# Kernel tuning notes

Measured on AMD Instinct MI355X. Metric: run time of the kernel, lower is better.

## Reference

```python
import jax, jax.numpy as jnp
import numpy as np

# Fixed hyperparameters from init_kwargs
KH, KW = 3, 3
GRID_SIZE = 5
SPLINE_ORDER = 3
GRID_RANGE = (-1.0, 1.0)


def _make_grid():
    # grid buffer: arange(-k, grid_size + k + 1) * h + grid_range[0], shape (G + 2k + 1,) = (12,)
    h = (GRID_RANGE[1] - GRID_RANGE[0]) / GRID_SIZE
    return (jnp.arange(-SPLINE_ORDER, GRID_SIZE + SPLINE_ORDER + 1, dtype=jnp.float32) * h
            + GRID_RANGE[0])


def _unfold(x):
    # torch.nn.Unfold with kernel (3,3), stride 1, pad 0, dilation 1.
    # Returns (N, C*KH*KW) with channel-major ordering (c, i, j), matching torch.
    B, C, H, W = x.shape
    Ho, Wo = H - KH + 1, W - KW + 1
    cols = [x[:, :, i:i + Ho, j:j + Wo] for i in range(KH) for j in range(KW)]
    p = jnp.stack(cols, axis=2)                    # (B, C, KH*KW, Ho, Wo)
    p = p.reshape(B, C * KH * KW, Ho * Wo)         # (B, in_features, L)
    p = p.transpose(0, 2, 1).reshape(-1, C * KH * KW)  # (B*L, in_features)
    return p, Ho, Wo


def _b_splines(x, grid):
    # x: (N, in_features); grid: (G + 2k + 1,) uniform, shared across features.
    # Returns (N, in_features, G + k) B-spline basis via Cox-de Boor recursion.
    x = x[..., None]  # (N, in, 1)
    bases = ((x >= grid[:-1]) & (x < grid[1:])).astype(x.dtype)  # (N, in, G+2k)
    for k in range(1, SPLINE_ORDER + 1):
        left = (x - grid[: -(k + 1)]) / (grid[k:-1] - grid[: -(k + 1)])
        right = (grid[k + 1:] - x) / (grid[k + 1:] - grid[1:-k])
        bases = left * bases[..., :-1] + right * bases[..., 1:]
    return bases  # (N, in, G + k)


def setup_inputs() -> dict:
    key = jax.random.key(0)
    k1, k2, k3, k4 = jax.random.split(key, 4)
    in_features = 32 * KH * KW  # 288
    out_features = 64
    n_coef = GRID_SIZE + SPLINE_ORDER  # 8
    x = jax.random.normal(k1, (16, 32, 64, 64), dtype=jnp.float32)
    base_weight = jax.random.normal(k2, (out_features, in_features), dtype=jnp.float32) * (1.0 / np.sqrt(in_features))
    spline_weight = jax.random.normal(k3, (out_features, in_features, n_coef), dtype=jnp.float32) * 0.1
    spline_scaler = jax.random.normal(k4, (out_features, in_features), dtype=jnp.float32) * (1.0 / np.sqrt(in_features))
    return {"x": x, "base_weight": base_weight, "spline_weight": spline_weight,
            "spline_scaler": spline_scaler}


def reference(x, base_weight, spline_weight, spline_scaler):
    B = x.shape[0]
    out_features = base_weight.shape[0]
    grid = _make_grid()

    patches, Ho, Wo = _unfold(x)                              # (N, in_features)
    N, in_features = patches.shape

    # KANLinear forward
    base_out = jnp.matmul(jax.nn.relu(patches), base_weight.T)  # (N, out)
    bases = _b_splines(patches, grid)                           # (N, in, G+k)
    scaled_w = spline_weight * spline_scaler[..., None]         # (out, in, G+k)
    spline_out = jnp.matmul(bases.reshape(N, -1), scaled_w.reshape(out_features, -1).T)
    out = base_out + spline_out                                 # (N, out)

    out = out.reshape(B, Ho, Wo, out_features).transpose(0, 3, 1, 2)  # (B, C_out, Ho, Wo)
    return out
```

## Files before the change

### kernel.cpp

```cpp
#include <hip/hip_runtime.h>
#include <stdint.h>

typedef _Float16 half8  __attribute__((ext_vector_type(8)));
typedef float    f32x4  __attribute__((ext_vector_type(4)));
typedef uint32_t u32x4  __attribute__((ext_vector_type(4)));

#define FIN  288
#define NOUT 64
#define LPB  3844
#define KSPL 72
#define SC   200
#define LDSN (31*SC + 2*64 + 64 + 8)


__global__ void prep_bfrag(const float* __restrict__ bw,
                           const float* __restrict__ sw,
                           const float* __restrict__ sc,
                           half8* __restrict__ bfrag) {
  int t = blockIdx.x * 256 + threadIdx.x;
  half8 v;
  int dst;
  if (t < NOUT * FIN) {
    int o = t / FIN;
    int f = t - o * FIN;
    float scale = sc[t];
    const float* p = sw + t * 8;
#pragma unroll
    for (int c = 0; c < 8; ++c) v[c] = (_Float16)(p[c] * scale);
    int ch = f / 9;
    int r  = f - ch * 9;
    int ii = r / 3;
    int jj = r - ii * 3;
    int g  = ch >> 2, q = ch & 3;
    int kt = ii * 24 + jj * 8 + g;
    dst = (kt * 4 + (o >> 4)) * 64 + q * 16 + (o & 15);
  } else {
    int t2 = t - NOUT * FIN;
    int lane = t2 & 63;
    int nf = (t2 >> 6) & 3;
    int ktb = t2 >> 8;
    int o = nf * 16 + (lane & 15);
    int f0 = ktb * 32 + (lane >> 4) * 8;
    const float* p = bw + o * FIN + f0;
#pragma unroll
    for (int c = 0; c < 8; ++c) v[c] = (_Float16)p[c];
    dst = ((KSPL + ktb) * 4 + nf) * 64 + lane;
  }
  bfrag[dst] = v;
}

__device__ inline half8 bspline8(float xv) {
  float u = fmaf(xv, 2.5f, 5.5f);
  float fi = floorf(u);
  int i = (int)fi;
  float t = u - fi, s = 1.0f - t;
  float t2 = t * t, t3 = t2 * t;
  float s2 = s * s, s3 = s2 * s;
  float w3 = t3 * 0.16666667f;
  float w0 = s3 * 0.16666667f;
  float w1 = fmaf(0.5f, t3, -t2) + 0.66666667f;
  float w2 = fmaf(0.5f, s3, -s2) + 0.66666667f;
  uint32_t u01 = __builtin_bit_cast(uint32_t, __builtin_amdgcn_cvt_pkrtz(w0, w1));
  uint32_t u23 = __builtin_bit_cast(uint32_t, __builtin_amdgcn_cvt_pkrtz(w2, w3));
  uint64_t V = (uint64_t)u01 | ((uint64_t)u23 << 32);
  uint32_t vl = (uint32_t)(V << 16);
  u32x4 fr;
#pragma unroll
  for (int q = 0; q < 4; ++q) {
    int d = i - 2 * q;
    uint32_t rr = (uint32_t)(V >> ((48 - 16 * d) & 63));
    fr[q] = ((uint32_t)d <= 3u) ? rr : ((d == 4) ? vl : 0u);
  }
  return __builtin_bit_cast(half8, fr);
}

__global__ __launch_bounds__(256, 4) void kan_main(
    const float* __restrict__ x,
    const half8* __restrict__ bfrag,
    float* __restrict__ out) {
  __shared__ float lx[LDSN];

  const int tid = threadIdx.x;
  const int bid = blockIdx.x;
  const int b  = bid / 62;
  const int ho = bid - b * 62;

  const float* xb = x + b * 131072 + ho * 64;
#pragma unroll
  for (int r = 0; r < 6; ++r) {
    int gid = r * 256 + tid;
    int row = gid >> 4;
    int c   = (row * 683) >> 11;
    int ii  = row - c * 3;
    int colv = (gid & 15) * 4;
    const float4 v = *(const float4*)(xb + c * 4096 + ii * 64 + colv);
    *(float4*)(&lx[c * SC + ii * 64 + colv]) = v;
  }
  __syncthreads();

  const int lane = tid & 63;
  const int wv   = tid >> 6;
  const int quad = lane >> 4;
  const int m16  = lane & 15;
  const int wo   = wv * 16 + m16;

  f32x4 acc[4];
#pragma unroll
  for (int nf = 0; nf < 4; ++nf) acc[nf] = (f32x4){0.f, 0.f, 0.f, 0.f};

  int kt = 0;
#pragma unroll
  for (int ii = 0; ii < 3; ++ii) {
#pragma unroll
    for (int jj = 0; jj < 3; ++jj) {
      const float* lbase = lx + quad * SC + ii * 64 + wo + jj;
#pragma unroll
      for (int g = 0; g < 8; ++g) {
        float xv = lbase[g * (4 * SC)];
        half8 af = bspline8(xv);
#pragma unroll
        for (int nf = 0; nf < 4; ++nf) {
          half8 bf = bfrag[(kt * 4 + nf) * 64 + lane];
          acc[nf] = __builtin_amdgcn_mfma_f32_16x16x32_f16(af, bf, acc[nf], 0, 0, 0);
        }
        ++kt;
      }
    }
  }

#pragma unroll
  for (int kb = 0; kb < 9; ++kb) {
    int f0 = kb * 32 + quad * 8;
    half8 a;
#pragma unroll
    for (int j = 0; j < 8; ++j) {
      int f = f0 + j;
      int c = (f * 57) >> 9;
      int r = f - c * 9;
      int i2 = (r * 11) >> 5;
      int j2 = r - i2 * 3;
      a[j] = (_Float16)fmaxf(lx[c * SC + i2 * 64 + wo + j2], 0.0f);
    }
#pragma unroll
    for (int nf = 0; nf < 4; ++nf) {
      half8 bf = bfrag[((KSPL + kb) * 4 + nf) * 64 + lane];
      acc[nf] = __builtin_amdgcn_mfma_f32_16x16x32_f16(a, bf, acc[nf], 0, 0, 0);
    }
  }

  float* ob = out + b * (NOUT * LPB) + ho * 62;
#pragma unroll
  for (int rg = 0; rg < 4; ++rg) {
    int wo2 = wv * 16 + quad * 4 + rg;
    if (wo2 < 62) {
#pragma unroll
      for (int nf = 0; nf < 4; ++nf) {
        int o = nf * 16 + m16;
        ob[o * LPB + wo2] = acc[nf][rg];
      }
    }
  }
}

extern "C" void kernel_launch(void* const* d_in, const int* in_sizes, int n_in,
                              void* d_out, int out_size, void* d_ws, size_t ws_size,
                              hipStream_t stream) {
  const float* x  = (const float*)d_in[0];
  const float* bw = (const float*)d_in[1];
  const float* sw = (const float*)d_in[2];
  const float* sc = (const float*)d_in[3];
  float* out = (float*)d_out;
  half8* bfrag = (half8*)d_ws;

  prep_bfrag<<<81, 256, 0, stream>>>(bw, sw, sc, bfrag);
  kan_main<<<16 * 62, 256, 0, stream>>>(x, bfrag, out);
}
```

Measured before the change: 121.3 us.

## Precompute B-spline bases in a separate pass and restructure GEMM with 32x32 MFMA tiles

Adds a kernel that evaluates the cubic B-spline basis once per input element and writes the half8 results to workspace. The main kernel is rewritten as a 128-pixel-tile GEMM using 32x32x16 MFMAs with weights as the A operand. Weight chunks are double-buffered in LDS through global_load_lds, and the basis vectors are read directly from global memory. This removes the nine-fold redundant basis evaluation per pixel, but adds a 32 MB intermediate write and read plus an extra launch. The grid also shrinks to 481 blocks of 128 threads, which may underfill the device.

New measurement: 145.3 us. 19.8% more time.

```diff
diff --git a/kernel.cpp b/kernel.cpp
--- a/kernel.cpp
+++ b/kernel.cpp
@@ -2,51 +2,51 @@
 #include <stdint.h>
 
 typedef _Float16 half8  __attribute__((ext_vector_type(8)));
-typedef float    f32x4  __attribute__((ext_vector_type(4)));
+typedef float    f32x16 __attribute__((ext_vector_type(16)));
 typedef uint32_t u32x4  __attribute__((ext_vector_type(4)));
 
-#define FIN  288
+#define NPIX 61504
+#define LPB  3844
 #define NOUT 64
-#define LPB  3844
-#define KSPL 72
-#define SC   200
-#define LDSN (31*SC + 2*64 + 64 + 8)
-
-
-__global__ void prep_bfrag(const float* __restrict__ bw,
-                           const float* __restrict__ sw,
-                           const float* __restrict__ sc,
-                           half8* __restrict__ bfrag) {
+#define NXPIX 2097152
+#define WTAB_HALF8 20736
+#define BFRAG_BYTES 332800
+#define WS_NEED ((size_t)BFRAG_BYTES + (size_t)NXPIX * 16)
+
+
+__global__ void prep_w(const float* __restrict__ bw,
+                       const float* __restrict__ sw,
+                       const float* __restrict__ sc,
+                       half8* __restrict__ wt) {
   int t = blockIdx.x * 256 + threadIdx.x;
   half8 v;
-  int dst;
-  if (t < NOUT * FIN) {
-    int o = t / FIN;
-    int f = t - o * FIN;
+  int fi, h, o;
+  if (t < 64 * 288) {
+    o = t / 288;
+    int f = t - o * 288;
     float scale = sc[t];
     const float* p = sw + t * 8;
 #pragma unroll
-    for (int c = 0; c < 8; ++c) v[c] = (_Float16)(p[c] * scale);
-    int ch = f / 9;
-    int r  = f - ch * 9;
-    int ii = r / 3;
-    int jj = r - ii * 3;
-    int g  = ch >> 2, q = ch & 3;
-    int kt = ii * 24 + jj * 8 + g;
-    dst = (kt * 4 + (o >> 4)) * 64 + q * 16 + (o & 15);
+    for (int j = 0; j < 8; ++j) v[j] = (_Float16)(p[j] * scale);
+    int c  = (f * 57) >> 9;
+    int r  = f - c * 9;
+    int i2 = (r * 11) >> 5;
+    int j2 = r - i2 * 3;
+    int st = (i2 * 3 + j2) * 16 + (c >> 1);
+    h  = c & 1;
+    fi = st * 2 + (o >> 5);
   } else {
-    int t2 = t - NOUT * FIN;
-    int lane = t2 & 63;
-    int nf = (t2 >> 6) & 3;
-    int ktb = t2 >> 8;
-    int o = nf * 16 + (lane & 15);
-    int f0 = ktb * 32 + (lane >> 4) * 8;
-    const float* p = bw + o * FIN + f0;
-#pragma unroll
-    for (int c = 0; c < 8; ++c) v[c] = (_Float16)p[c];
-    dst = ((KSPL + ktb) * 4 + nf) * 64 + lane;
-  }
-  bfrag[dst] = v;
+    int t2 = t - 64 * 288;
+    o = t2 / 36;
+    int g8 = t2 - o * 36;
+    const float* p = bw + o * 288 + g8 * 8;
+#pragma unroll
+    for (int j = 0; j < 8; ++j) v[j] = (_Float16)p[j];
+    int stb = g8 >> 1;
+    h  = g8 & 1;
+    fi = (144 + stb) * 2 + (o >> 5);
+  }
+  wt[fi * 64 + h * 32 + (o & 31)] = v;
 }
 
 __device__ inline half8 bspline8(float xv) {
@@ -74,91 +74,148 @@
   return __builtin_bit_cast(half8, fr);
 }
 
-__global__ __launch_bounds__(256, 4) void kan_main(
+__global__ void precompute_basis(const float* __restrict__ x,
+                                 half8* __restrict__ bsp) {
+  int i = blockIdx.x * 256 + threadIdx.x;
+  bsp[i] = bspline8(x[i]);
+}
+
+__device__ inline void stage_chunk(const half8* __restrict__ s, half8* d,
+                                   int nhalf8, int lane) {
+  for (int it = 0; it < nhalf8; it += 64) {
+#if __has_builtin(__builtin_amdgcn_global_load_lds)
+    __builtin_amdgcn_global_load_lds(
+        (const __attribute__((address_space(1))) uint32_t*)(s + it + lane),
+        (__attribute__((address_space(3))) uint32_t*)(d + it),
+        16, 0, 0);
+#else
+    d[it + lane] = s[it + lane];
+#endif
+  }
+}
+
+__global__ __launch_bounds__(128) void kan_main3(
     const float* __restrict__ x,
-    const half8* __restrict__ bfrag,
+    const half8* __restrict__ bsp,
+    const half8* __restrict__ wt,
     float* __restrict__ out) {
-  __shared__ float lx[LDSN];
-
-  const int tid = threadIdx.x;
-  const int bid = blockIdx.x;
-  const int b  = bid / 62;
-  const int ho = bid - b * 62;
-
-  const float* xb = x + b * 131072 + ho * 64;
-#pragma unroll
-  for (int r = 0; r < 6; ++r) {
-    int gid = r * 256 + tid;
-    int row = gid >> 4;
-    int c   = (row * 683) >> 11;
-    int ii  = row - c * 3;
-    int colv = (gid & 15) * 4;
-    const float4 v = *(const float4*)(xb + c * 4096 + ii * 64 + colv);
-    *(float4*)(&lx[c * SC + ii * 64 + colv]) = v;
-  }
-  __syncthreads();
-
+  __shared__ half8 smw[2][2048];
+
+  const int tid  = threadIdx.x;
   const int lane = tid & 63;
   const int wv   = tid >> 6;
-  const int quad = lane >> 4;
-  const int m16  = lane & 15;
-  const int wo   = wv * 16 + m16;
-
-  f32x4 acc[4];
-#pragma unroll
-  for (int nf = 0; nf < 4; ++nf) acc[nf] = (f32x4){0.f, 0.f, 0.f, 0.f};
-
-  int kt = 0;
-#pragma unroll
-  for (int ii = 0; ii < 3; ++ii) {
-#pragma unroll
-    for (int jj = 0; jj < 3; ++jj) {
-      const float* lbase = lx + quad * SC + ii * 64 + wo + jj;
-#pragma unroll
-      for (int g = 0; g < 8; ++g) {
-        float xv = lbase[g * (4 * SC)];
-        half8 af = bspline8(xv);
-#pragma unroll
-        for (int nf = 0; nf < 4; ++nf) {
-          half8 bf = bfrag[(kt * 4 + nf) * 64 + lane];
-          acc[nf] = __builtin_amdgcn_mfma_f32_16x16x32_f16(af, bf, acc[nf], 0, 0, 0);
+  const int l31  = lane & 31;
+  const int h    = lane >> 5;
+
+  int bid  = blockIdx.x;
+  int tile = (bid < 480) ? ((bid & 7) * 60 + (bid >> 3)) : 480;
+  const int pxw = tile * 128 + wv * 64;
+
+  int xb[2];
+#pragma unroll
+  for (int np = 0; np < 2; ++np) {
+    int p = pxw + np * 32 + l31;
+    if (p > NPIX - 1) p = NPIX - 1;
+    int b  = p / LPB;
+    int l  = p - b * LPB;
+    int ho = l / 62;
+    int wo = l - ho * 62;
+    xb[np] = b * 131072 + ho * 64 + wo;
+  }
+
+  f32x16 acc[2][2];
+#pragma unroll
+  for (int mo = 0; mo < 2; ++mo)
+#pragma unroll
+    for (int np = 0; np < 2; ++np)
+#pragma unroll
+      for (int i = 0; i < 16; ++i) acc[mo][np][i] = 0.f;
+
+  stage_chunk(wt + 0, &smw[0][0] + wv * 1024 - wv * 1024 + wv * 1024, 0, 0);
+  stage_chunk(wt + wv * 1024, &smw[0][wv * 1024], 1024, lane);
+
+  int buf = 0;
+  for (int ch = 0; ch < 11; ++ch) {
+    __syncthreads();
+    if (ch < 10) {
+      int nfr  = (ch < 9) ? 2048 : 256;
+      int half = ((ch + 1 < 10) ? 2048 : 256) >> 1;
+      (void)nfr;
+      stage_chunk(wt + (ch + 1) * 2048 + wv * half, &smw[buf ^ 1][wv * half],
+                  half, lane);
+    }
+    const half8* wb = &smw[buf][0];
+
+    if (ch < 9) {
+      int i2 = (ch * 11) >> 5;
+      int j2 = ch - i2 * 3;
+      const half8* bp0 = bsp + xb[0] + h * 4096 + i2 * 64 + j2;
+      const half8* bp1 = bsp + xb[1] + h * 4096 + i2 * 64 + j2;
+#pragma unroll
+      for (int stl = 0; stl < 16; ++stl) {
+        half8 b0 = bp0[stl * 8192];
+        half8 b1 = bp1[stl * 8192];
+        half8 a0 = wb[stl * 128 + lane];
+        half8 a1 = wb[stl * 128 + 64 + lane];
+        acc[0][0] = __builtin_amdgcn_mfma_f32_32x32x16_f16(a0, b0, acc[0][0], 0, 0, 0);
+        acc[0][1] = __builtin_amdgcn_mfma_f32_32x32x16_f16(a0, b1, acc[0][1], 0, 0, 0);
+        acc[1][0] = __builtin_amdgcn_mfma_f32_32x32x16_f16(a1, b0, acc[1][0], 0, 0, 0);
+        acc[1][1] = __builtin_amdgcn_mfma_f32_32x32x16_f16(a1, b1, acc[1][1], 0, 0, 0);
+      }
+    } else {
+      int nst = (ch == 9) ? 16 : 2;
+      for (int stl = 0; stl < nst; ++stl) {
+        int stb = (ch - 9) * 16 + stl;
+        int fb0 = stb * 16 + h * 8;
+        half8 bb[2];
+#pragma unroll
+        for (int np = 0; np < 2; ++np) {
+          u32x4 pk;
+#pragma unroll
+          for (int jj = 0; jj < 4; ++jj) {
+            float v0, v1;
+            {
+              int f = fb0 + jj * 2;
+              int c = (f * 57) >> 9; int r = f - c * 9;
+              int a = (r * 11) >> 5; int b2 = r - a * 3;
+              v0 = fmaxf(x[xb[np] + c * 4096 + a * 64 + b2], 0.f);
+            }
+            {
+              int f = fb0 + jj * 2 + 1;
+              int c = (f * 57) >> 9; int r = f - c * 9;
+              int a = (r * 11) >> 5; int b2 = r - a * 3;
+              v1 = fmaxf(x[xb[np] + c * 4096 + a * 64 + b2], 0.f);
+            }
+            pk[jj] = __builtin_bit_cast(uint32_t, __builtin_amdgcn_cvt_pkrtz(v0, v1));
+          }
+          bb[np] = __builtin_bit_cast(half8, pk);
         }
-        ++kt;
+        half8 a0 = wb[stl * 128 + lane];
+        half8 a1 = wb[stl * 128 + 64 + lane];
+        acc[0][0] = __builtin_amdgcn_mfma_f32_32x32x16_f16(a0, bb[0], acc[0][0], 0, 0, 0);
+        acc[0][1] = __builtin_amdgcn_mfma_f32_32x32x16_f16(a0, bb[1], acc[0][1], 0, 0, 0);
+        acc[1][0] = __builtin_amdgcn_mfma_f32_32x32x16_f16(a1, bb[0], acc[1][0], 0, 0, 0);
+        acc[1][1] = __builtin_amdgcn_mfma_f32_32x32x16_f16(a1, bb[1], acc[1][1], 0, 0, 0);
       }
     }
-  }
-
-#pragma unroll
-  for (int kb = 0; kb < 9; ++kb) {
-    int f0 = kb * 32 + quad * 8;
-    half8 a;
-#pragma unroll
-    for (int j = 0; j < 8; ++j) {
-      int f = f0 + j;
-      int c = (f * 57) >> 9;
-      int r = f - c * 9;
-      int i2 = (r * 11) >> 5;
-      int j2 = r - i2 * 3;
-      a[j] = (_Float16)fmaxf(lx[c * SC + i2 * 64 + wo + j2], 0.0f);
-    }
-#pragma unroll
-    for (int nf = 0; nf < 4; ++nf) {
-      half8 bf = bfrag[((KSPL + kb) * 4 + nf) * 64 + lane];
-      acc[nf] = __builtin_amdgcn_mfma_f32_16x16x32_f16(a, bf, acc[nf], 0, 0, 0);
-    }
-  }
-
-  float* ob = out + b * (NOUT * LPB) + ho * 62;
-#pragma unroll
-  for (int rg = 0; rg < 4; ++rg) {
-    int wo2 = wv * 16 + quad * 4 + rg;
-    if (wo2 < 62) {
-#pragma unroll
-      for (int nf = 0; nf < 4; ++nf) {
-        int o = nf * 16 + m16;
-        ob[o * LPB + wo2] = acc[nf][rg];
+    buf ^= 1;
+  }
+
+#pragma unroll
+  for (int np = 0; np < 2; ++np) {
+    int p = pxw + np * 32 + l31;
+    bool ok = p < NPIX;
+    int pc = ok ? p : NPIX - 1;
+    int b = pc / LPB;
+    int l = pc - b * LPB;
+    float* ob = out + b * (NOUT * LPB) + l;
+#pragma unroll
+    for (int mo = 0; mo < 2; ++mo)
+#pragma unroll
+      for (int rg = 0; rg < 16; ++rg) {
+        int o = mo * 32 + (rg & 3) + 8 * (rg >> 2) + 4 * h;
+        if (ok) ob[o * LPB] = acc[mo][np][rg];
       }
-    }
   }
 }
 
@@ -170,8 +227,10 @@
   const float* sw = (const float*)d_in[2];
   const float* sc = (const float*)d_in[3];
   float* out = (float*)d_out;
-  half8* bfrag = (half8*)d_ws;
-
-  prep_bfrag<<<81, 256, 0, stream>>>(bw, sw, sc, bfrag);
-  kan_main<<<16 * 62, 256, 0, stream>>>(x, bfrag, out);
-}
+  half8* wt  = (half8*)d_ws;
+  half8* bsp = (half8*)((char*)d_ws + BFRAG_BYTES);
+
+  prep_w<<<81, 256, 0, stream>>>(bw, sw, sc, wt);
+  precompute_basis<<<NXPIX / 256, 256, 0, stream>>>(x, bsp);
+  kan_main3<<<481, 128, 0, stream>>>(x, bsp, wt, out);
+}
```
